# Optimization experiments

Hardware: AMD Instinct MI355X
Metric: run time of the kernel (lower is better)

## Reference

```python
import jax, jax.numpy as jnp
import numpy as np

N = 50000
E = 800000
EPS = 1e-12


def sage_conv(x, src, dst, W_l, b_l, W_r):
    # PyG SAGEConv (mean aggr): out = lin_l(mean_{j in N(i)} x_j) + lin_r(x_i)
    msg = x[src]                                             # [E, d] gather
    agg = jax.ops.segment_sum(msg, dst, num_segments=N)      # [N, d]
    cnt = jax.ops.segment_sum(jnp.ones((E,), x.dtype), dst, num_segments=N)
    mean = agg / jnp.maximum(cnt, 1.0)[:, None]              # isolated nodes -> 0
    return mean @ W_l + b_l + x @ W_r


def setup_inputs() -> dict:
    key = jax.random.key(0)
    ks = jax.random.split(key, 12)
    s = 0.05
    return {
        "x": jax.random.normal(ks[0], (N, 128), dtype=jnp.float32),
        "edge_index": jax.random.randint(ks[1], (2, E), 0, N, dtype=jnp.int64),
        # pre: Linear(128 -> 128)
        "pre_W": jax.random.normal(ks[2], (128, 128), dtype=jnp.float32) * s,
        "pre_b": jnp.zeros((128,), dtype=jnp.float32),
        # conv_first: SAGEConv(128 -> 256)
        "W1_l": jax.random.normal(ks[3], (128, 256), dtype=jnp.float32) * s,
        "b1": jnp.zeros((256,), dtype=jnp.float32),
        "W1_r": jax.random.normal(ks[4], (128, 256), dtype=jnp.float32) * s,
        # conv_hidden[0]: SAGEConv(256 -> 256)
        "W2_l": jax.random.normal(ks[5], (256, 256), dtype=jnp.float32) * s,
        "b2": jnp.zeros((256,), dtype=jnp.float32),
        "W2_r": jax.random.normal(ks[6], (256, 256), dtype=jnp.float32) * s,
        # conv_out: SAGEConv(256 -> 256)
        "W3_l": jax.random.normal(ks[7], (256, 256), dtype=jnp.float32) * s,
        "b3": jnp.zeros((256,), dtype=jnp.float32),
        "W3_r": jax.random.normal(ks[8], (256, 256), dtype=jnp.float32) * s,
    }


def reference(x, edge_index, pre_W, pre_b, W1_l, b1, W1_r, W2_l, b2, W2_r, W3_l, b3, W3_r):
    src, dst = edge_index[0], edge_index[1]
    h = x @ pre_W + pre_b                                   # feature_pre Linear
    h = jax.nn.relu(sage_conv(h, src, dst, W1_l, b1, W1_r))  # dropout = identity (eval)
    h = jax.nn.relu(sage_conv(h, src, dst, W2_l, b2, W2_r))
    h = sage_conv(h, src, dst, W3_l, b3, W3_r)
    norm = jnp.sqrt(jnp.sum(h * h, axis=-1, keepdims=True))
    return h / jnp.maximum(norm, EPS)                       # F.normalize(p=2, dim=-1)
```

## Files before the change

### kernel.cpp

```cpp
#include <hip/hip_runtime.h>
#include <cstddef>
#include <cstdint>


typedef __attribute__((ext_vector_type(8))) short short8;
typedef __attribute__((ext_vector_type(4))) float f32x4;

__device__ __forceinline__ unsigned rne_bf16(float f) {
    unsigned b = __float_as_uint(f);
    return (b + 0x7fffu + ((b >> 16) & 1u)) >> 16;
}
__device__ __forceinline__ float bf16_lo(unsigned u) { return __uint_as_float(u << 16); }
__device__ __forceinline__ float bf16_hi(unsigned u) { return __uint_as_float(u & 0xffff0000u); }


__global__ __launch_bounds__(256) void deg_kernel(const int* __restrict__ dst,
                                                  int* __restrict__ deg, int E) {
    int e = blockIdx.x * 256 + threadIdx.x;
    if (e < E) atomicAdd(&deg[dst[e]], 1);
}

__global__ __launch_bounds__(256) void bsum_kernel(const int* __restrict__ deg,
                                                   int* __restrict__ bsum, int n) {
    int i = blockIdx.x * 256 + threadIdx.x;
    int v = (i < n) ? deg[i] : 0;
#pragma unroll
    for (int s = 32; s > 0; s >>= 1) v += __shfl_down(v, s);
    __shared__ int ws[4];
    int lane = threadIdx.x & 63, w = threadIdx.x >> 6;
    if (lane == 0) ws[w] = v;
    __syncthreads();
    if (threadIdx.x == 0) bsum[blockIdx.x] = ws[0] + ws[1] + ws[2] + ws[3];
}

__global__ __launch_bounds__(256) void bscan_kernel(const int* __restrict__ bsum,
                                                    int* __restrict__ boff,
                                                    int* __restrict__ off,
                                                    int nb, int n, int E) {
    int t = threadIdx.x;
    int v = (t < nb) ? bsum[t] : 0;
    int incl = v;
#pragma unroll
    for (int s = 1; s < 64; s <<= 1) {
        int u = __shfl_up(incl, s);
        if ((t & 63) >= s) incl += u;
    }
    __shared__ int ws[4];
    int lane = t & 63, w = t >> 6;
    if (lane == 63) ws[w] = incl;
    __syncthreads();
    int woff = 0;
    for (int j = 0; j < w; ++j) woff += ws[j];
    if (t < nb) boff[t] = woff + incl - v;
    if (t == 0) off[n] = E;
}

__global__ __launch_bounds__(256) void scan_kernel(const int* __restrict__ deg,
                                                   const int* __restrict__ boff,
                                                   int* __restrict__ off,
                                                   float* __restrict__ inv, int n) {
    int i = blockIdx.x * 256 + threadIdx.x;
    int v = (i < n) ? deg[i] : 0;
    int incl = v;
#pragma unroll
    for (int s = 1; s < 64; s <<= 1) {
        int u = __shfl_up(incl, s);
        if ((threadIdx.x & 63) >= s) incl += u;
    }
    __shared__ int ws[4];
    int lane = threadIdx.x & 63, w = threadIdx.x >> 6;
    if (lane == 63) ws[w] = incl;
    __syncthreads();
    int woff = 0;
    for (int j = 0; j < w; ++j) woff += ws[j];
    if (i < n) {
        off[i] = boff[blockIdx.x] + woff + incl - v;
        inv[i] = 1.0f / fmaxf((float)v, 1.0f);
    }
}

__global__ __launch_bounds__(256) void fill_kernel(const int* __restrict__ src,
                                                   const int* __restrict__ dst,
                                                   const int* __restrict__ off,
                                                   int* __restrict__ deg,
                                                   int* __restrict__ ssrc, int E) {
    int e = blockIdx.x * 256 + threadIdx.x;
    if (e >= E) return;
    int d = dst[e];
    int pos = off[d] + atomicSub(&deg[d], 1) - 1;
    ssrc[pos] = src[e];
}


__global__ __launch_bounds__(256) void xconv(const float* __restrict__ x,
                                             uint2* __restrict__ xb, int n4) {
    int i = blockIdx.x * 256 + threadIdx.x;
    if (i >= n4) return;
    float4 v = ((const float4*)x)[i];
    uint2 o;
    o.x = rne_bf16(v.x) | (rne_bf16(v.y) << 16);
    o.y = rne_bf16(v.z) | (rne_bf16(v.w) << 16);
    xb[i] = o;
}

__global__ __launch_bounds__(256) void wprep(
    const float* __restrict__ pre_W, const float* __restrict__ W1_l,
    const float* __restrict__ W1_r, const float* __restrict__ W2_l,
    const float* __restrict__ W2_r, const float* __restrict__ W3_l,
    const float* __restrict__ W3_r,
    unsigned short* __restrict__ WT0, unsigned short* __restrict__ WT1,
    unsigned short* __restrict__ WT2, unsigned short* __restrict__ WT3,
    unsigned short* __restrict__ WT4, unsigned short* __restrict__ WT5,
    unsigned short* __restrict__ WT6) {
    int idx = blockIdx.x * 256 + threadIdx.x;
    if (idx < 16384) {
        int k = idx >> 7, n = idx & 127;
        WT0[n * 128 + k] = (unsigned short)rne_bf16(pre_W[idx]);
        return;
    }
    idx -= 16384;
    if (idx < 32768) {
        int k = idx >> 8, n = idx & 255;
        WT1[n * 128 + k] = (unsigned short)rne_bf16(W1_l[idx]);
        return;
    }
    idx -= 32768;
    if (idx < 32768) {
        int k = idx >> 8, n = idx & 255;
        WT2[n * 128 + k] = (unsigned short)rne_bf16(W1_r[idx]);
        return;
    }
    idx -= 32768;
    if (idx < 65536) {
        int k = idx >> 8, n = idx & 255;
        WT3[n * 256 + k] = (unsigned short)rne_bf16(W2_l[idx]);
        return;
    }
    idx -= 65536;
    if (idx < 65536) {
        int k = idx >> 8, n = idx & 255;
        WT4[n * 256 + k] = (unsigned short)rne_bf16(W2_r[idx]);
        return;
    }
    idx -= 65536;
    if (idx < 65536) {
        int k = idx >> 8, n = idx & 255;
        WT5[n * 256 + k] = (unsigned short)rne_bf16(W3_l[idx]);
        return;
    }
    idx -= 65536;
    if (idx < 65536) {
        int k = idx >> 8, n = idx & 255;
        WT6[n * 256 + k] = (unsigned short)rne_bf16(W3_r[idx]);
    }
}


template <int D>
__global__ __launch_bounds__(256) void gather_b(const unsigned short* __restrict__ h,
                                                const int* __restrict__ off,
                                                const int* __restrict__ ssrc,
                                                const float* __restrict__ inv,
                                                unsigned short* __restrict__ agg, int n) {
    int node = blockIdx.x * 4 + (threadIdx.x >> 6);
    if (node >= n) return;
    int lane = threadIdx.x & 63;
    int beg = off[node], end = off[node + 1];
    float sc = inv[node];

    if (D == 256) {
        const int half = lane >> 5;
        const int sub  = lane & 31;
        const unsigned short* col = h + (sub << 3);
        float a[8] = {0, 0, 0, 0, 0, 0, 0, 0};
        float b[8] = {0, 0, 0, 0, 0, 0, 0, 0};
        int k = beg;
        for (; k + 3 < end; k += 4) {
            int s0 = ssrc[k + half];
            int s1 = ssrc[k + 2 + half];
            uint4 u = *(const uint4*)(col + (size_t)s0 * 256);
            uint4 v = *(const uint4*)(col + (size_t)s1 * 256);
            a[0] += bf16_lo(u.x); a[1] += bf16_hi(u.x);
            a[2] += bf16_lo(u.y); a[3] += bf16_hi(u.y);
            a[4] += bf16_lo(u.z); a[5] += bf16_hi(u.z);
            a[6] += bf16_lo(u.w); a[7] += bf16_hi(u.w);
            b[0] += bf16_lo(v.x); b[1] += bf16_hi(v.x);
            b[2] += bf16_lo(v.y); b[3] += bf16_hi(v.y);
            b[4] += bf16_lo(v.z); b[5] += bf16_hi(v.z);
            b[6] += bf16_lo(v.w); b[7] += bf16_hi(v.w);
        }
        for (; k < end; k += 2) {
            int e = k + half;
            if (e < end) {
                uint4 u = *(const uint4*)(col + (size_t)ssrc[e] * 256);
                a[0] += bf16_lo(u.x); a[1] += bf16_hi(u.x);
                a[2] += bf16_lo(u.y); a[3] += bf16_hi(u.y);
                a[4] += bf16_lo(u.z); a[5] += bf16_hi(u.z);
                a[6] += bf16_lo(u.w); a[7] += bf16_hi(u.w);
            }
        }
#pragma unroll
        for (int i = 0; i < 8; ++i) a[i] += b[i];
#pragma unroll
        for (int i = 0; i < 8; ++i) a[i] += __shfl_xor(a[i], 32);
        if (half == 0) {
#pragma unroll
            for (int i = 0; i < 8; ++i) a[i] *= sc;
            uint4 o;
            o.x = rne_bf16(a[0]) | (rne_bf16(a[1]) << 16);
            o.y = rne_bf16(a[2]) | (rne_bf16(a[3]) << 16);
            o.z = rne_bf16(a[4]) | (rne_bf16(a[5]) << 16);
            o.w = rne_bf16(a[6]) | (rne_bf16(a[7]) << 16);
            *(uint4*)(agg + (size_t)node * 256 + (sub << 3)) = o;
        }
    } else {
        const int q   = lane >> 4;
        const int sub = lane & 15;
        const unsigned short* col = h + (sub << 3);
        float a[8] = {0, 0, 0, 0, 0, 0, 0, 0};
        float b[8] = {0, 0, 0, 0, 0, 0, 0, 0};
        int k = beg;
        for (; k + 7 < end; k += 8) {
            int s0 = ssrc[k + q];
            int s1 = ssrc[k + 4 + q];
            uint4 u = *(const uint4*)(col + (size_t)s0 * 128);
            uint4 v = *(const uint4*)(col + (size_t)s1 * 128);
            a[0] += bf16_lo(u.x); a[1] += bf16_hi(u.x);
            a[2] += bf16_lo(u.y); a[3] += bf16_hi(u.y);
            a[4] += bf16_lo(u.z); a[5] += bf16_hi(u.z);
            a[6] += bf16_lo(u.w); a[7] += bf16_hi(u.w);
            b[0] += bf16_lo(v.x); b[1] += bf16_hi(v.x);
            b[2] += bf16_lo(v.y); b[3] += bf16_hi(v.y);
            b[4] += bf16_lo(v.z); b[5] += bf16_hi(v.z);
            b[6] += bf16_lo(v.w); b[7] += bf16_hi(v.w);
        }
        for (; k < end; k += 4) {
            int e = k + q;
            if (e < end) {
                uint4 u = *(const uint4*)(col + (size_t)ssrc[e] * 128);
                a[0] += bf16_lo(u.x); a[1] += bf16_hi(u.x);
                a[2] += bf16_lo(u.y); a[3] += bf16_hi(u.y);
                a[4] += bf16_lo(u.z); a[5] += bf16_hi(u.z);
                a[6] += bf16_lo(u.w); a[7] += bf16_hi(u.w);
            }
        }
#pragma unroll
        for (int i = 0; i < 8; ++i) a[i] += b[i];
#pragma unroll
        for (int i = 0; i < 8; ++i) a[i] += __shfl_xor(a[i], 16);
#pragma unroll
        for (int i = 0; i < 8; ++i) a[i] += __shfl_xor(a[i], 32);
        if (q == 0) {
#pragma unroll
            for (int i = 0; i < 8; ++i) a[i] *= sc;
            uint4 o;
            o.x = rne_bf16(a[0]) | (rne_bf16(a[1]) << 16);
            o.y = rne_bf16(a[2]) | (rne_bf16(a[3]) << 16);
            o.z = rne_bf16(a[4]) | (rne_bf16(a[5]) << 16);
            o.w = rne_bf16(a[6]) | (rne_bf16(a[7]) << 16);
            *(uint4*)(agg + (size_t)node * 128 + (sub << 3)) = o;
        }
    }
}

__global__ __launch_bounds__(256) void gemm_bt(
    const unsigned short* __restrict__ A1, const unsigned short* __restrict__ W1T,
    const unsigned short* __restrict__ A2, const unsigned short* __restrict__ W2T,
    const float* __restrict__ bias,
    unsigned short* __restrict__ outb, float* __restrict__ outf,
    int M, int K, int Nn, int relu) {
    __shared__ __align__(16) unsigned short As[128 * 64];
    __shared__ __align__(16) unsigned short Bs[128 * 64];

    const int t = threadIdx.x;
    const int lane = t & 63;
    const int w = t >> 6;
    const int wm = w >> 1, wn = w & 1;
    const int m0 = blockIdx.x * 128;
    const int n0 = blockIdx.y * 128;

    f32x4 acc[4][4];
#pragma unroll
    for (int i = 0; i < 4; ++i)
#pragma unroll
        for (int j = 0; j < 4; ++j) acc[i][j] = (f32x4){0.f, 0.f, 0.f, 0.f};

    for (int pass = 0; pass < 2; ++pass) {
        const unsigned short* A = pass ? A2 : A1;
        const unsigned short* W = pass ? W2T : W1T;
        if (pass && A2 == nullptr) break;

        for (int k0 = 0; k0 < K; k0 += 64) {
#pragma unroll
            for (int r = 0; r < 4; ++r) {
                int p = r * 256 + t;
                int row = p >> 3, slot = p & 7;
                int c = slot ^ (row & 7);
                int gm = m0 + row;
                if (gm >= M) gm = M - 1;
                uint4 va = *(const uint4*)(A + (size_t)gm * K + k0 + c * 8);
                uint4 vb = *(const uint4*)(W + (size_t)(n0 + row) * K + k0 + c * 8);
                *(uint4*)&As[(size_t)p * 8] = va;
                *(uint4*)&Bs[(size_t)p * 8] = vb;
            }
            __syncthreads();
#pragma unroll
            for (int kk = 0; kk < 2; ++kk) {
                short8 af[4], bfr[4];
                int ac = kk * 4 + (lane >> 4);
#pragma unroll
                for (int i = 0; i < 4; ++i) {
                    int arow = wm * 64 + i * 16 + (lane & 15);
                    af[i] = *(const short8*)&As[arow * 64 + ((ac ^ (arow & 7)) << 3)];
                    int brow = wn * 64 + i * 16 + (lane & 15);
                    bfr[i] = *(const short8*)&Bs[brow * 64 + ((ac ^ (brow & 7)) << 3)];
                }
#pragma unroll
                for (int mi = 0; mi < 4; ++mi)
#pragma unroll
                    for (int ni = 0; ni < 4; ++ni)
                        acc[mi][ni] = __builtin_amdgcn_mfma_f32_16x16x32_bf16(
                            af[mi], bfr[ni], acc[mi][ni], 0, 0, 0);
            }
            __syncthreads();
        }
    }

#pragma unroll
    for (int ni = 0; ni < 4; ++ni) {
        int n = n0 + wn * 64 + ni * 16 + (lane & 15);
        float bv = (bias != nullptr) ? bias[n] : 0.0f;
#pragma unroll
        for (int mi = 0; mi < 4; ++mi) {
            int mbase = m0 + wm * 64 + mi * 16 + ((lane >> 4) << 2);
#pragma unroll
            for (int r = 0; r < 4; ++r) {
                int m = mbase + r;
                if (m >= M) continue;
                float v = acc[mi][ni][r] + bv;
                if (relu) v = fmaxf(v, 0.0f);
                if (outb) outb[(size_t)m * Nn + n] = (unsigned short)rne_bf16(v);
                else      outf[(size_t)m * Nn + n] = v;
            }
        }
    }
}

__global__ __launch_bounds__(256) void norm_kernel(float* __restrict__ out, int M) {
    int row  = blockIdx.x * 4 + (threadIdx.x >> 6);
    int lane = threadIdx.x & 63;
    if (row >= M) return;
    float4 v = *(float4*)(out + (size_t)row * 256 + (lane << 2));
    float s = v.x * v.x + v.y * v.y + v.z * v.z + v.w * v.w;
#pragma unroll
    for (int off = 32; off > 0; off >>= 1) s += __shfl_down(s, off);
    s = __shfl(s, 0);
    float scale = 1.0f / fmaxf(sqrtf(s), 1e-12f);
    v.x *= scale; v.y *= scale; v.z *= scale; v.w *= scale;
    *(float4*)(out + (size_t)row * 256 + (lane << 2)) = v;
}

extern "C" void kernel_launch(void* const* d_in, const int* in_sizes, int n_in,
                              void* d_out, int out_size, void* d_ws, size_t ws_size,
                              hipStream_t stream) {
    const int N = 50000;
    const int E = 800000;
    const int NB = (N + 255) / 256;

    const float* x     = (const float*)d_in[0];
    const int*   ei    = (const int*)d_in[1];
    const float* pre_W = (const float*)d_in[2];
    const float* pre_b = (const float*)d_in[3];
    const float* W1_l  = (const float*)d_in[4];
    const float* b1    = (const float*)d_in[5];
    const float* W1_r  = (const float*)d_in[6];
    const float* W2_l  = (const float*)d_in[7];
    const float* b2    = (const float*)d_in[8];
    const float* W2_r  = (const float*)d_in[9];
    const float* W3_l  = (const float*)d_in[10];
    const float* b3    = (const float*)d_in[11];
    const float* W3_r  = (const float*)d_in[12];
    float* out = (float*)d_out;

    const int* src = ei;
    const int* dst = ei + E;

    int* deg  = (int*)d_ws;
    int* off  = deg + N;
    int* bsum = off + N + 1;
    int* boff = bsum + 256;
    int* ssrc = boff + 256;
    size_t int_words = (size_t)2 * N + 1 + 512 + E;
    int_words = (int_words + 3) & ~(size_t)3;

    float* inv = (float*)d_ws + int_words;
    unsigned short* us = (unsigned short*)(inv + N);

    unsigned short* xb  = us;                 us += (size_t)N * 128;
    unsigned short* WT0 = us;                 us += 16384;
    unsigned short* WT1 = us;                 us += 32768;
    unsigned short* WT2 = us;                 us += 32768;
    unsigned short* WT3 = us;                 us += 65536;
    unsigned short* WT4 = us;                 us += 65536;
    unsigned short* WT5 = us;                 us += 65536;
    unsigned short* WT6 = us;                 us += 65536;
    unsigned short* h0b   = us;               us += (size_t)N * 128;
    unsigned short* agg1b = us;               us += (size_t)N * 128;
    unsigned short* h1b   = us;               us += (size_t)N * 256;
    unsigned short* agg2b = us;               us += (size_t)N * 256;
    unsigned short* h2b   = us;               us += (size_t)N * 256;
    unsigned short* agg3b = us;               us += (size_t)N * 256;

    hipMemsetAsync(deg, 0, (size_t)N * sizeof(int), stream);
    deg_kernel<<<(E + 255) / 256, 256, 0, stream>>>(dst, deg, E);
    bsum_kernel<<<NB, 256, 0, stream>>>(deg, bsum, N);
    bscan_kernel<<<1, 256, 0, stream>>>(bsum, boff, off, NB, N, E);
    scan_kernel<<<NB, 256, 0, stream>>>(deg, boff, off, inv, N);
    fill_kernel<<<(E + 255) / 256, 256, 0, stream>>>(src, dst, off, deg, ssrc, E);

    xconv<<<(N * 128 / 4 + 255) / 256, 256, 0, stream>>>(x, (uint2*)xb, N * 128 / 4);
    wprep<<<(344064 + 255) / 256, 256, 0, stream>>>(pre_W, W1_l, W1_r, W2_l, W2_r,
                                                    W3_l, W3_r, WT0, WT1, WT2, WT3,
                                                    WT4, WT5, WT6);

    const int MT = (N + 127) / 128;
    const int AG = (N + 3) / 4;

    gemm_bt<<<dim3(MT, 1), 256, 0, stream>>>(xb, WT0, nullptr, nullptr, pre_b,
                                             h0b, nullptr, N, 128, 128, 0);

    gather_b<128><<<AG, 256, 0, stream>>>(h0b, off, ssrc, inv, agg1b, N);
    gemm_bt<<<dim3(MT, 2), 256, 0, stream>>>(agg1b, WT1, h0b, WT2, b1,
                                             h1b, nullptr, N, 128, 256, 1);

    gather_b<256><<<AG, 256, 0, stream>>>(h1b, off, ssrc, inv, agg2b, N);
    gemm_bt<<<dim3(MT, 2), 256, 0, stream>>>(agg2b, WT3, h1b, WT4, b2,
                                             h2b, nullptr, N, 256, 256, 1);

    gather_b<256><<<AG, 256, 0, stream>>>(h2b, off, ssrc, inv, agg3b, N);
    gemm_bt<<<dim3(MT, 2), 256, 0, stream>>>(agg3b, WT5, h2b, WT6, b3,
                                             nullptr, out, N, 256, 256, 0);

    norm_kernel<<<AG, 256, 0, stream>>>(out, N);
}
```

Before: 520.7 us.

## Widen SAGE GEMMs to full 256 columns, fuse L2 normalize, merge prep kernels

Adds a 512-thread GEMM kernel that computes all 256 output columns per 128-row tile. It loads each A tile once instead of twice and stages tiles with global_load_lds direct-to-LDS copies. The final layer's row L2 normalization is fused into the GEMM epilogue through a shared-memory row-sum reduction, which removes the separate norm kernel and a full fp32 read/write of the output. The x conversion and weight prep kernels are merged into one launch. The cost is a larger LDS footprint (48KB+) and bigger blocks, which may lower occupancy.

```diff
diff --git a/kernel.cpp b/kernel.cpp
--- a/kernel.cpp
+++ b/kernel.cpp
@@ -12,6 +12,18 @@
 }
 __device__ __forceinline__ float bf16_lo(unsigned u) { return __uint_as_float(u << 16); }
 __device__ __forceinline__ float bf16_hi(unsigned u) { return __uint_as_float(u & 0xffff0000u); }
+
+__device__ __forceinline__ void stage16(const void* g, unsigned short* ldsbase,
+                                        int lane) {
+#if __has_builtin(__builtin_amdgcn_global_load_lds)
+    (void)lane;
+    __builtin_amdgcn_global_load_lds(
+        (const __attribute__((address_space(1))) unsigned int*)g,
+        (__attribute__((address_space(3))) unsigned int*)ldsbase, 16, 0, 0);
+#else
+    *(uint4*)(ldsbase + (size_t)lane * 8) = *(const uint4*)g;
+#endif
+}
 
 
 __global__ __launch_bounds__(256) void deg_kernel(const int* __restrict__ dst,
@@ -92,18 +104,8 @@
 }
 
 
-__global__ __launch_bounds__(256) void xconv(const float* __restrict__ x,
-                                             uint2* __restrict__ xb, int n4) {
-    int i = blockIdx.x * 256 + threadIdx.x;
-    if (i >= n4) return;
-    float4 v = ((const float4*)x)[i];
-    uint2 o;
-    o.x = rne_bf16(v.x) | (rne_bf16(v.y) << 16);
-    o.y = rne_bf16(v.z) | (rne_bf16(v.w) << 16);
-    xb[i] = o;
-}
-
-__global__ __launch_bounds__(256) void wprep(
+__global__ __launch_bounds__(256) void prep_all(
+    const float* __restrict__ x, uint2* __restrict__ xb, int n4, int XB,
     const float* __restrict__ pre_W, const float* __restrict__ W1_l,
     const float* __restrict__ W1_r, const float* __restrict__ W2_l,
     const float* __restrict__ W2_r, const float* __restrict__ W3_l,
@@ -112,7 +114,17 @@
     unsigned short* __restrict__ WT2, unsigned short* __restrict__ WT3,
     unsigned short* __restrict__ WT4, unsigned short* __restrict__ WT5,
     unsigned short* __restrict__ WT6) {
-    int idx = blockIdx.x * 256 + threadIdx.x;
+    if (blockIdx.x < (unsigned)XB) {
+        int i = blockIdx.x * 256 + threadIdx.x;
+        if (i >= n4) return;
+        float4 v = ((const float4*)x)[i];
+        uint2 o;
+        o.x = rne_bf16(v.x) | (rne_bf16(v.y) << 16);
+        o.y = rne_bf16(v.z) | (rne_bf16(v.w) << 16);
+        xb[i] = o;
+        return;
+    }
+    int idx = (blockIdx.x - XB) * 256 + threadIdx.x;
     if (idx < 16384) {
         int k = idx >> 7, n = idx & 127;
         WT0[n * 128 + k] = (unsigned short)rne_bf16(pre_W[idx]);
@@ -265,10 +277,8 @@
 
 __global__ __launch_bounds__(256) void gemm_bt(
     const unsigned short* __restrict__ A1, const unsigned short* __restrict__ W1T,
-    const unsigned short* __restrict__ A2, const unsigned short* __restrict__ W2T,
-    const float* __restrict__ bias,
-    unsigned short* __restrict__ outb, float* __restrict__ outf,
-    int M, int K, int Nn, int relu) {
+    const float* __restrict__ bias, unsigned short* __restrict__ outb,
+    int M, int K, int Nn) {
     __shared__ __align__(16) unsigned short As[128 * 64];
     __shared__ __align__(16) unsigned short Bs[128 * 64];
 
@@ -285,23 +295,102 @@
 #pragma unroll
         for (int j = 0; j < 4; ++j) acc[i][j] = (f32x4){0.f, 0.f, 0.f, 0.f};
 
+    for (int k0 = 0; k0 < K; k0 += 64) {
+#pragma unroll
+        for (int r = 0; r < 4; ++r) {
+            int p = r * 256 + t;
+            int row = p >> 3, slot = p & 7;
+            int c = slot ^ (row & 7);
+            int gm = m0 + row;
+            if (gm >= M) gm = M - 1;
+            uint4 va = *(const uint4*)(A1 + (size_t)gm * K + k0 + c * 8);
+            uint4 vb = *(const uint4*)(W1T + (size_t)(n0 + row) * K + k0 + c * 8);
+            *(uint4*)&As[(size_t)p * 8] = va;
+            *(uint4*)&Bs[(size_t)p * 8] = vb;
+        }
+        __syncthreads();
+#pragma unroll
+        for (int kk = 0; kk < 2; ++kk) {
+            short8 af[4], bfr[4];
+            int ac = kk * 4 + (lane >> 4);
+#pragma unroll
+            for (int i = 0; i < 4; ++i) {
+                int arow = wm * 64 + i * 16 + (lane & 15);
+                af[i] = *(const short8*)&As[arow * 64 + ((ac ^ (arow & 7)) << 3)];
+                int brow = wn * 64 + i * 16 + (lane & 15);
+                bfr[i] = *(const short8*)&Bs[brow * 64 + ((ac ^ (brow & 7)) << 3)];
+            }
+#pragma unroll
+            for (int mi = 0; mi < 4; ++mi)
+#pragma unroll
+                for (int ni = 0; ni < 4; ++ni)
+                    acc[mi][ni] = __builtin_amdgcn_mfma_f32_16x16x32_bf16(
+                        af[mi], bfr[ni], acc[mi][ni], 0, 0, 0);
+        }
+        __syncthreads();
+    }
+
+#pragma unroll
+    for (int ni = 0; ni < 4; ++ni) {
+        int n = n0 + wn * 64 + ni * 16 + (lane & 15);
+        float bv = (bias != nullptr) ? bias[n] : 0.0f;
+#pragma unroll
+        for (int mi = 0; mi < 4; ++mi) {
+            int mbase = m0 + wm * 64 + mi * 16 + ((lane >> 4) << 2);
+#pragma unroll
+            for (int r = 0; r < 4; ++r) {
+                int m = mbase + r;
+                if (m >= M) continue;
+                outb[(size_t)m * Nn + n] = (unsigned short)rne_bf16(acc[mi][ni][r] + bv);
+            }
+        }
+    }
+}
+
+__global__ __launch_bounds__(512) void gemm_wide(
+    const unsigned short* __restrict__ A1, const unsigned short* __restrict__ W1T,
+    const unsigned short* __restrict__ A2, const unsigned short* __restrict__ W2T,
+    const float* __restrict__ bias,
+    unsigned short* __restrict__ outb, float* __restrict__ outf,
+    int M, int K, int relu) {
+    __shared__ __align__(16) unsigned short As[128 * 64];
+    __shared__ __align__(16) unsigned short Bs[256 * 64];
+    __shared__ float rs[128][4];
+
+    const int t = threadIdx.x;
+    const int lane = t & 63;
+    const int w8 = t >> 6;
+    const int wm = w8 >> 2, wn = w8 & 3;
+    const int m0 = blockIdx.x * 128;
+
+    f32x4 acc[4][4];
+#pragma unroll
+    for (int i = 0; i < 4; ++i)
+#pragma unroll
+        for (int j = 0; j < 4; ++j) acc[i][j] = (f32x4){0.f, 0.f, 0.f, 0.f};
+
     for (int pass = 0; pass < 2; ++pass) {
         const unsigned short* A = pass ? A2 : A1;
         const unsigned short* W = pass ? W2T : W1T;
-        if (pass && A2 == nullptr) break;
 
         for (int k0 = 0; k0 < K; k0 += 64) {
 #pragma unroll
-            for (int r = 0; r < 4; ++r) {
-                int p = r * 256 + t;
+            for (int i = 0; i < 2; ++i) {
+                int base = (w8 * 2 + i) * 64;
+                int p = base + lane;
                 int row = p >> 3, slot = p & 7;
                 int c = slot ^ (row & 7);
                 int gm = m0 + row;
                 if (gm >= M) gm = M - 1;
-                uint4 va = *(const uint4*)(A + (size_t)gm * K + k0 + c * 8);
-                uint4 vb = *(const uint4*)(W + (size_t)(n0 + row) * K + k0 + c * 8);
-                *(uint4*)&As[(size_t)p * 8] = va;
-                *(uint4*)&Bs[(size_t)p * 8] = vb;
+                stage16(A + (size_t)gm * K + k0 + c * 8, &As[(size_t)base * 8], lane);
+            }
+#pragma unroll
+            for (int i = 0; i < 4; ++i) {
+                int base = (w8 * 4 + i) * 64;
+                int p = base + lane;
+                int row = p >> 3, slot = p & 7;
+                int c = slot ^ (row & 7);
+                stage16(W + (size_t)row * K + k0 + c * 8, &Bs[(size_t)base * 8], lane);
             }
             __syncthreads();
 #pragma unroll
@@ -326,38 +415,67 @@
         }
     }
 
+    if (outb) {
+#pragma unroll
+        for (int ni = 0; ni < 4; ++ni) {
+            int n = wn * 64 + ni * 16 + (lane & 15);
+            float bv = bias[n];
+#pragma unroll
+            for (int mi = 0; mi < 4; ++mi) {
+                int mbase = m0 + wm * 64 + mi * 16 + ((lane >> 4) << 2);
+#pragma unroll
+                for (int r = 0; r < 4; ++r) {
+                    int m = mbase + r;
+                    if (m >= M) continue;
+                    float v = acc[mi][ni][r] + bv;
+                    if (relu) v = fmaxf(v, 0.0f);
+                    outb[(size_t)m * 256 + n] = (unsigned short)rne_bf16(v);
+                }
+            }
+        }
+        return;
+    }
+
 #pragma unroll
     for (int ni = 0; ni < 4; ++ni) {
-        int n = n0 + wn * 64 + ni * 16 + (lane & 15);
-        float bv = (bias != nullptr) ? bias[n] : 0.0f;
-#pragma unroll
-        for (int mi = 0; mi < 4; ++mi) {
-            int mbase = m0 + wm * 64 + mi * 16 + ((lane >> 4) << 2);
-#pragma unroll
-            for (int r = 0; r < 4; ++r) {
-                int m = mbase + r;
-                if (m >= M) continue;
-                float v = acc[mi][ni][r] + bv;
-                if (relu) v = fmaxf(v, 0.0f);
-                if (outb) outb[(size_t)m * Nn + n] = (unsigned short)rne_bf16(v);
-                else      outf[(size_t)m * Nn + n] = v;
-            }
-        }
-    }
-}
-
-__global__ __launch_bounds__(256) void norm_kernel(float* __restrict__ out, int M) {
-    int row  = blockIdx.x * 4 + (threadIdx.x >> 6);
-    int lane = threadIdx.x & 63;
-    if (row >= M) return;
-    float4 v = *(float4*)(out + (size_t)row * 256 + (lane << 2));
-    float s = v.x * v.x + v.y * v.y + v.z * v.z + v.w * v.w;
-#pragma unroll
-    for (int off = 32; off > 0; off >>= 1) s += __shfl_down(s, off);
-    s = __shfl(s, 0);
-    float scale = 1.0f / fmaxf(sqrtf(s), 1e-12f);
-    v.x *= scale; v.y *= scale; v.z *= scale; v.w *= scale;
-    *(float4*)(out + (size_t)row * 256 + (lane << 2)) = v;
+        float bv = bias[wn * 64 + ni * 16 + (lane & 15)];
+#pragma unroll
+        for (int mi = 0; mi < 4; ++mi)
+#pragma unroll
+            for (int r = 0; r < 4; ++r) acc[mi][ni][r] += bv;
+    }
+#pragma unroll
+    for (int mi = 0; mi < 4; ++mi) {
+#pragma unroll
+        for (int r = 0; r < 4; ++r) {
+            float p = acc[mi][0][r] * acc[mi][0][r] + acc[mi][1][r] * acc[mi][1][r] +
+                      acc[mi][2][r] * acc[mi][2][r] + acc[mi][3][r] * acc[mi][3][r];
+            p += __shfl_xor(p, 1);
+            p += __shfl_xor(p, 2);
+            p += __shfl_xor(p, 4);
+            p += __shfl_xor(p, 8);
+            if ((lane & 15) == 0)
+                rs[wm * 64 + mi * 16 + ((lane >> 4) << 2) + r][wn] = p;
+        }
+    }
+    __syncthreads();
+#pragma unroll
+    for (int mi = 0; mi < 4; ++mi) {
+        int mbase = m0 + wm * 64 + mi * 16 + ((lane >> 4) << 2);
+        int lrow = wm * 64 + mi * 16 + ((lane >> 4) << 2);
+#pragma unroll
+        for (int r = 0; r < 4; ++r) {
+            int m = mbase + r;
+            if (m >= M) continue;
+            float s = rs[lrow + r][0] + rs[lrow + r][1] + rs[lrow + r][2] + rs[lrow + r][3];
+            float sc = 1.0f / fmaxf(sqrtf(s), 1e-12f);
+#pragma unroll
+            for (int ni = 0; ni < 4; ++ni) {
+                int n = wn * 64 + ni * 16 + (lane & 15);
+                outf[(size_t)m * 256 + n] = acc[mi][ni][r] * sc;
+            }
+        }
+    }
 }
 
 extern "C" void kernel_launch(void* const* d_in, const int* in_sizes, int n_in,
@@ -418,28 +536,27 @@
     scan_kernel<<<NB, 256, 0, stream>>>(deg, boff, off, inv, N);
     fill_kernel<<<(E + 255) / 256, 256, 0, stream>>>(src, dst, off, deg, ssrc, E);
 
-    xconv<<<(N * 128 / 4 + 255) / 256, 256, 0, stream>>>(x, (uint2*)xb, N * 128 / 4);
-    wprep<<<(344064 + 255) / 256, 256, 0, stream>>>(pre_W, W1_l, W1_r, W2_l, W2_r,
-                                                    W3_l, W3_r, WT0, WT1, WT2, WT3,
-                                                    WT4, WT5, WT6);
+    const int n4 = N * 128 / 4;
+    const int XB = (n4 + 255) / 256;
+    const int WB = (344064 + 255) / 256;
+    prep_all<<<XB + WB, 256, 0, stream>>>(x, (uint2*)xb, n4, XB,
+                                          pre_W, W1_l, W1_r, W2_l, W2_r, W3_l,
+                                          W3_r, WT0, WT1, WT2, WT3, WT4, WT5, WT6);
 
     const int MT = (N + 127) / 128;
     const int AG = (N + 3) / 4;
 
-    gemm_bt<<<dim3(MT, 1), 256, 0, stream>>>(xb, WT0, nullptr, nullptr, pre_b,
-                                             h0b, nullptr, N, 128, 128, 0);
+    gemm_bt<<<dim3(MT, 1), 256, 0, stream>>>(xb, WT0, pre_b, h0b, N, 128, 128);
 
     gather_b<128><<<AG, 256, 0, stream>>>(h0b, off, ssrc, inv, agg1b, N);
-    gemm_bt<<<dim3(MT, 2), 256, 0, stream>>>(agg1b, WT1, h0b, WT2, b1,
-                                             h1b, nullptr, N, 128, 256, 1);
+    gemm_wide<<<MT, 512, 0, stream>>>(agg1b, WT1, h0b, WT2, b1, h1b, nullptr,
+                                      N, 128, 1);
 
     gather_b<256><<<AG, 256, 0, stream>>>(h1b, off, ssrc, inv, agg2b, N);
-    gemm_bt<<<dim3(MT, 2), 256, 0, stream>>>(agg2b, WT3, h1b, WT4, b2,
-                                             h2b, nullptr, N, 256, 256, 1);
+    gemm_wide<<<MT, 512, 0, stream>>>(agg2b, WT3, h1b, WT4, b2, h2b, nullptr,
+                                      N, 256, 1);
 
     gather_b<256><<<AG, 256, 0, stream>>>(h2b, off, ssrc, inv, agg3b, N);
-    gemm_bt<<<dim3(MT, 2), 256, 0, stream>>>(agg3b, WT5, h2b, WT6, b3,
-                                             nullptr, out, N, 256, 256, 0);
-
-    norm_kernel<<<AG, 256, 0, stream>>>(out, N);
-}
+    gemm_wide<<<MT, 512, 0, stream>>>(agg3b, WT5, h2b, WT6, b3, nullptr, out,
+                                      N, 256, 0);
+}
```

New measurement: 497.1 us. 1.05x faster.
